# Kernel optimization log

Measured on AMD Instinct MI355X. Metric: run time of the kernel, lower is better.

Reference implementation:

```python
import jax, jax.numpy as jnp
import numpy as np

M = 12288
B = 1
C_IN = 8
C_OUT = 16
K = 5


def setup_inputs() -> dict:
    key = jax.random.key(0)
    kL, kx, kt = jax.random.split(key, 3)
    # Scale L so its spectral radius is ~0.5, keeping L^k x numerically tame.
    L = jax.random.normal(kL, (M, M), dtype=jnp.float32) * (0.5 / np.sqrt(M))
    x = jax.random.normal(kx, (B, C_IN, M), dtype=jnp.float32)
    theta = jax.random.normal(kt, (C_OUT, C_IN, K), dtype=jnp.float32)
    bias = jnp.zeros((1, C_OUT, 1), dtype=jnp.float32)
    return {"L": L, "x": x, "theta": theta, "bias": bias}


def reference(L, x, theta, bias):
    Bb, C_in, Mm = x.shape
    Kk = theta.shape[-1]
    # Batch the shared recurrence L^k x into one (M,M)x(M,B*C_in) matmul per step.
    cur = x.reshape(Bb * C_in, Mm).T          # [M, B*C_in]
    powers = [cur]
    for _ in range(Kk - 1):                   # small fixed K, structural loop
        cur = L @ cur                         # [M, B*C_in]
        powers.append(cur)
    X = jnp.stack(powers, axis=0)             # [K, M, B*C_in]
    X = X.transpose(2, 1, 0).reshape(Bb, C_in, Mm, Kk)  # [B, C_in, M, K]
    y = jnp.einsum('bimk,oik->bom', X, theta)           # [B, C_out, M]
    return y + bias
```

## Files before the change

kernel.cpp:

```cpp
#include <hip/hip_runtime.h>
#include <hip/hip_bf16.h>

#define MM 12288
#define NCH 8
#define COUT 16
#define KK 5
#define ROWS 4
#define WPB 8
#define RB (ROWS * WPB)
#define CHUNK 256

__global__ __launch_bounds__(512) void matpanel_kernel(
        const float* __restrict__ L,
        const float* __restrict__ vin,
        float* __restrict__ vout) {
    const int tid  = threadIdx.x;
    const int lane = tid & 63;
    const int wave = tid >> 6;
    const int row0 = blockIdx.x * RB + wave * ROWS;

    const int sc = wave;
    const int sj = lane * 4;

    __shared__ float sv[NCH][CHUNK];

    float acc[ROWS][NCH];
#pragma unroll
    for (int r = 0; r < ROWS; ++r)
#pragma unroll
        for (int c = 0; c < NCH; ++c) acc[r][c] = 0.f;

    for (int it = 0; it < MM / CHUNK; ++it) {
        const int jbase = it * CHUNK;

        const float4 t = *(const float4*)(vin + (size_t)sc * MM + jbase + sj);
        float4 la[ROWS];
#pragma unroll
        for (int r = 0; r < ROWS; ++r)
            la[r] = *(const float4*)(L + (size_t)(row0 + r) * MM + jbase + lane * 4);

        __syncthreads();
        *(float4*)(&sv[sc][sj]) = t;
        __syncthreads();

#pragma unroll
        for (int c = 0; c < NCH; ++c) {
            const float4 v = *(const float4*)(&sv[c][lane * 4]);
#pragma unroll
            for (int r = 0; r < ROWS; ++r) {
                acc[r][c] += la[r].x * v.x + la[r].y * v.y
                           + la[r].z * v.z + la[r].w * v.w;
            }
        }
    }

    float val[ROWS * NCH];
#pragma unroll
    for (int r = 0; r < ROWS; ++r)
#pragma unroll
        for (int c = 0; c < NCH; ++c) val[r * NCH + c] = acc[r][c];

#pragma unroll
    for (int v = 0; v < 32; ++v) val[v] += __shfl_xor(val[v], 32, 64);

#pragma unroll
    for (int d = 16; d >= 1; d >>= 1) {
        const bool up = (lane & d) != 0;
#pragma unroll
        for (int v = 0; v < 16; ++v) {
            if (v < d) {
                const float keep = up ? val[v + d] : val[v];
                const float send = up ? val[v] : val[v + d];
                const float recv = __shfl_xor(send, d, 64);
                val[v] = keep + recv;
            }
        }
    }

    if (lane < 32) {
        const int r = lane >> 3;
        const int c = lane & 7;
        vout[(size_t)c * MM + row0 + r] = val[0];
    }
}

__global__ __launch_bounds__(256) void combine_kernel(
        const float* __restrict__ x,
        const float* __restrict__ P,
        const float* __restrict__ theta,
        const float* __restrict__ bias,
        float* __restrict__ y) {
    const int m = blockIdx.x * blockDim.x + threadIdx.x;
    if (m >= MM) return;

    float p[KK][NCH];
#pragma unroll
    for (int c = 0; c < NCH; ++c) p[0][c] = x[(size_t)c * MM + m];
#pragma unroll
    for (int k = 1; k < KK; ++k)
#pragma unroll
        for (int c = 0; c < NCH; ++c)
            p[k][c] = P[((size_t)(k - 1) * NCH + c) * MM + m];

#pragma unroll
    for (int o = 0; o < COUT; ++o) {
        float acc = bias[o];
#pragma unroll
        for (int c = 0; c < NCH; ++c)
#pragma unroll
            for (int k = 0; k < KK; ++k)
                acc += theta[(o * NCH + c) * KK + k] * p[k][c];
        y[(size_t)o * MM + m] = acc;
    }
}

extern "C" void kernel_launch(void* const* d_in, const int* in_sizes, int n_in,
                              void* d_out, int out_size, void* d_ws, size_t ws_size,
                              hipStream_t stream) {
    const float* L     = (const float*)d_in[0];
    const float* x     = (const float*)d_in[1];
    const float* theta = (const float*)d_in[2];
    const float* bias  = (const float*)d_in[3];
    float* out = (float*)d_out;
    float* P   = (float*)d_ws;

    const size_t S = (size_t)NCH * MM;
    const int grid = MM / RB;

    matpanel_kernel<<<grid, 512, 0, stream>>>(L, x,         P);
    matpanel_kernel<<<grid, 512, 0, stream>>>(L, P,         P + S);
    matpanel_kernel<<<grid, 512, 0, stream>>>(L, P + S,     P + 2 * S);
    matpanel_kernel<<<grid, 512, 0, stream>>>(L, P + 2 * S, P + 3 * S);

    combine_kernel<<<(MM + 255) / 256, 256, 0, stream>>>(x, P, theta, bias, out);
}
```

Measured before the change: 1.200 ms.

## Double-buffer vector chunks and prefetch next L tile in matpanel kernel

Shrinks blocks from 8 to 4 waves and adds a double-buffered shared-memory vector tile, so each thread stages two channels. The next chunk of L and the vector is loaded into registers while the current chunk is being computed, and one barrier per iteration replaces two. The aim is to hide global-load latency on the memory-bound L stream, at the cost of more registers, which may lower occupancy. Grid size doubles, and each block reloads the shared vector for fewer rows.

```diff
diff --git a/kernel.cpp b/kernel.cpp
--- a/kernel.cpp
+++ b/kernel.cpp
@@ -6,11 +6,12 @@
 #define COUT 16
 #define KK 5
 #define ROWS 4
-#define WPB 8
+#define WPB 4
 #define RB (ROWS * WPB)
 #define CHUNK 256
+#define NIT (MM / CHUNK)
 
-__global__ __launch_bounds__(512) void matpanel_kernel(
+__global__ __launch_bounds__(256) void matpanel_kernel(
         const float* __restrict__ L,
         const float* __restrict__ vin,
         float* __restrict__ vout) {
@@ -19,10 +20,10 @@
     const int wave = tid >> 6;
     const int row0 = blockIdx.x * RB + wave * ROWS;
 
-    const int sc = wave;
-    const int sj = lane * 4;
+    const int sch  = tid >> 6;
+    const int scol = (tid & 63) * 4;
 
-    __shared__ float sv[NCH][CHUNK];
+    __shared__ float sv[2][NCH][CHUNK];
 
     float acc[ROWS][NCH];
 #pragma unroll
@@ -30,28 +31,44 @@
 #pragma unroll
         for (int c = 0; c < NCH; ++c) acc[r][c] = 0.f;
 
-    for (int it = 0; it < MM / CHUNK; ++it) {
-        const int jbase = it * CHUNK;
+    float4 t0 = *(const float4*)(vin + (size_t)sch * MM + scol);
+    float4 t1 = *(const float4*)(vin + (size_t)(sch + 4) * MM + scol);
+    float4 la[ROWS];
+#pragma unroll
+    for (int r = 0; r < ROWS; ++r)
+        la[r] = *(const float4*)(L + (size_t)(row0 + r) * MM + lane * 4);
 
-        const float4 t = *(const float4*)(vin + (size_t)sc * MM + jbase + sj);
-        float4 la[ROWS];
+    int p = 0;
+#pragma unroll 2
+    for (int it = 0; it < NIT; ++it) {
+        *(float4*)(&sv[p][sch][scol])     = t0;
+        *(float4*)(&sv[p][sch + 4][scol]) = t1;
+        __syncthreads();
+
+        const int itn   = (it + 1 < NIT) ? (it + 1) : it;
+        const int jnext = itn * CHUNK;
+        float4 t0n = *(const float4*)(vin + (size_t)sch * MM + jnext + scol);
+        float4 t1n = *(const float4*)(vin + (size_t)(sch + 4) * MM + jnext + scol);
+        float4 lan[ROWS];
 #pragma unroll
         for (int r = 0; r < ROWS; ++r)
-            la[r] = *(const float4*)(L + (size_t)(row0 + r) * MM + jbase + lane * 4);
-
-        __syncthreads();
-        *(float4*)(&sv[sc][sj]) = t;
-        __syncthreads();
+            lan[r] = *(const float4*)(L + (size_t)(row0 + r) * MM + jnext + lane * 4);
 
 #pragma unroll
         for (int c = 0; c < NCH; ++c) {
-            const float4 v = *(const float4*)(&sv[c][lane * 4]);
+            const float4 v = *(const float4*)(&sv[p][c][lane * 4]);
 #pragma unroll
             for (int r = 0; r < ROWS; ++r) {
                 acc[r][c] += la[r].x * v.x + la[r].y * v.y
                            + la[r].z * v.z + la[r].w * v.w;
             }
         }
+
+#pragma unroll
+        for (int r = 0; r < ROWS; ++r) la[r] = lan[r];
+        t0 = t0n;
+        t1 = t1n;
+        p ^= 1;
     }
 
     float val[ROWS * NCH];
@@ -127,10 +144,10 @@
     const size_t S = (size_t)NCH * MM;
     const int grid = MM / RB;
 
-    matpanel_kernel<<<grid, 512, 0, stream>>>(L, x,         P);
-    matpanel_kernel<<<grid, 512, 0, stream>>>(L, P,         P + S);
-    matpanel_kernel<<<grid, 512, 0, stream>>>(L, P + S,     P + 2 * S);
-    matpanel_kernel<<<grid, 512, 0, stream>>>(L, P + 2 * S, P + 3 * S);
+    matpanel_kernel<<<grid, 256, 0, stream>>>(L, x,         P);
+    matpanel_kernel<<<grid, 256, 0, stream>>>(L, P,         P + S);
+    matpanel_kernel<<<grid, 256, 0, stream>>>(L, P + S,     P + 2 * S);
+    matpanel_kernel<<<grid, 256, 0, stream>>>(L, P + 2 * S, P + 3 * S);
 
     combine_kernel<<<(MM + 255) / 256, 256, 0, stream>>>(x, P, theta, bias, out);
 }
```

Result: faster. 1.159 ms (-3.4%).
